# Performance work log

Hardware: AMD Instinct MI355X
Metric: run time of the kernel (lower is better)

Reference implementation:

```python
import jax, jax.numpy as jnp
import numpy as np

D = 6            # tree depth: 63 nodes per tree, leaves-first level order
HL = 256         # lstm hidden dim
HM = 128         # mlp hid dim
OFFSETS = [0, 32, 48, 56, 60, 62]  # level l occupies [off, off+2**(D-1-l))


def _lin(k, fan_in, fan_out, scale=0.02):
    return jax.random.normal(k, (fan_in, fan_out), jnp.float32) * scale


def setup_inputs() -> dict:
    key = jax.random.key(0)
    ks = jax.random.split(key, 40)
    B, N = 1024, 63
    inp = {
        "op": jax.random.normal(ks[0], (B, N, 32), jnp.float32),
        "feat": jax.random.normal(ks[1], (B, N, 64), jnp.float32),
        "cond1": jax.random.normal(ks[2], (B, N, 256), jnp.float32),
        "cond2": jax.random.normal(ks[3], (B, N, 256), jnp.float32),
        "bitmap": jax.random.uniform(ks[4], (B, N, 1000), jnp.float32),
        "has_cond": jnp.ones((B, N), jnp.float32),
        # embeddings (stored [in, out], i.e. transposed torch Linear weight)
        "W_op": _lin(ks[5], 32, HM), "b_op": jnp.zeros((HM,), jnp.float32),
        "W_feat": _lin(ks[6], 64, HM), "b_feat": jnp.zeros((HM,), jnp.float32),
        "W_pred": _lin(ks[7], 256, HM), "b_pred": jnp.zeros((HM,), jnp.float32),
        "W_bm": _lin(ks[8], 1000, HM), "b_bm": jnp.zeros((HM,), jnp.float32),
        # node LSTM (torch layout: [4*HL, in])
        "W_ih": jax.random.normal(ks[9], (4 * HL, 5 * HM), jnp.float32) * 0.02,
        "b_ih": jnp.zeros((4 * HL,), jnp.float32),
        "W_hh": jax.random.normal(ks[10], (4 * HL, HL), jnp.float32) * 0.02,
        "b_hh": jnp.zeros((4 * HL,), jnp.float32),
        # descendant attention
        "W_wh": _lin(ks[11], HL, 64), "W_ext": _lin(ks[12], 5 * HM, 64),
        "W_a": _lin(ks[13], 64, 1),
        "W_ht": _lin(ks[14], HL, HL), "b_ht": jnp.zeros((HL,), jnp.float32),
        # output heads
        "W_c1": _lin(ks[15], HL, HM), "b_c1": jnp.zeros((HM,), jnp.float32),
        "W_c2": _lin(ks[16], HM, HM), "b_c2": jnp.zeros((HM,), jnp.float32),
        "W_c3": _lin(ks[17], HM, 1), "b_c3": jnp.zeros((1,), jnp.float32),
        "W_d1": _lin(ks[18], HL, HM), "b_d1": jnp.zeros((HM,), jnp.float32),
        "W_d2": _lin(ks[19], HM, HM), "b_d2": jnp.zeros((HM,), jnp.float32),
        "W_d3": _lin(ks[20], HM, 1), "b_d3": jnp.zeros((1,), jnp.float32),
    }
    return inp


def _tree_forward(op, feat, cond1, cond2, bitmap, has_cond,
                  W_op, b_op, W_feat, b_feat, W_pred, b_pred, W_bm, b_bm,
                  W_ih, b_ih, W_hh, b_hh, W_wh, W_ext, W_a, W_ht, b_ht):
    B = op.shape[0]
    # per-node 5*HM input vector (conditions are single Compare predicates)
    x = jnp.concatenate([
        op @ W_op + b_op,
        feat @ W_feat + b_feat,
        cond1 @ W_pred + b_pred,
        cond2 @ W_pred + b_pred,
        (bitmap @ W_bm + b_bm) * has_cond[..., None],
    ], axis=-1)                                        # [B, 63, 5*HM]

    hiddens, cells = [], []
    for l in range(D):
        n, off = 2 ** (D - 1 - l), OFFSETS[l]
        xl = x[:, off:off + n]                         # [B, n, 5*HM]
        if l == 0:  # leaves: no children, no descendants
            h0 = jnp.zeros((B, n, HL), x.dtype)
            c0 = h0
        else:
            # all descendant hiddens of each node, grouped per parent
            desc = jnp.concatenate(
                [hiddens[lp].reshape(B, n, 2 ** (l - lp), HL) for lp in range(l)],
                axis=2)                                # [B, n, M, HL]
            e = jnp.tanh(desc @ W_wh + (xl @ W_ext)[:, :, None, :])
            logits = (e @ W_a)[..., 0]                 # [B, n, M]
            w = jax.nn.softmax(logits, axis=-1)        # exp/sum(exp)
            pooled = jnp.einsum('bnm,bnmh->bnh', w, desc)
            h0 = jnp.tanh(pooled @ W_ht + b_ht)        # hidden_transformation
            c0 = 0.5 * cells[l - 1].reshape(B, n, 2, HL).sum(axis=2)  # avg child cells
        # single-step LSTM (torch gate order i, f, g, o)
        gates = xl @ W_ih.T + b_ih + h0 @ W_hh.T + b_hh
        i_, f_, g_, o_ = jnp.split(gates, 4, axis=-1)
        c = jax.nn.sigmoid(f_) * c0 + jax.nn.sigmoid(i_) * jnp.tanh(g_)
        h = jax.nn.sigmoid(o_) * jnp.tanh(c)
        hiddens.append(h)
        cells.append(c)
    return hiddens[-1][:, 0]                           # root hidden [B, HL]


def reference(op, feat, cond1, cond2, bitmap, has_cond,
              W_op, b_op, W_feat, b_feat, W_pred, b_pred, W_bm, b_bm,
              W_ih, b_ih, W_hh, b_hh, W_wh, W_ext, W_a, W_ht, b_ht,
              W_c1, b_c1, W_c2, b_c2, W_c3, b_c3,
              W_d1, b_d1, W_d2, b_d2, W_d3, b_d3):
    root = _tree_forward(op, feat, cond1, cond2, bitmap, has_cond,
                         W_op, b_op, W_feat, b_feat, W_pred, b_pred, W_bm, b_bm,
                         W_ih, b_ih, W_hh, b_hh, W_wh, W_ext, W_a, W_ht, b_ht)
    cost = jax.nn.sigmoid(jax.nn.relu(jax.nn.relu(root @ W_c1 + b_c1) @ W_c2 + b_c2) @ W_c3 + b_c3)
    card = jax.nn.sigmoid(jax.nn.relu(jax.nn.relu(root @ W_d1 + b_d1) @ W_d2 + b_d2) @ W_d3 + b_d3)
    return (cost, card)
```

## Files before the change

kernel.cpp:

```cpp
#include <hip/hip_runtime.h>
#include <math.h>

typedef unsigned short u16;
typedef __bf16 bf16x8 __attribute__((ext_vector_type(8)));
typedef float f32x4 __attribute__((ext_vector_type(4)));

static __device__ __forceinline__ float sigf(float x){ return 1.0f/(1.0f+expf(-x)); }
static __device__ __forceinline__ u16 f2bf(float f){
    unsigned u = __builtin_bit_cast(unsigned, f);
    unsigned r = u + 0x7FFFu + ((u >> 16) & 1u);
    return (u16)(r >> 16);
}
static __device__ __forceinline__ float b2f(u16 s){
    unsigned u = ((unsigned)s) << 16;
    return __builtin_bit_cast(float, u);
}

__global__ void prep_w(const float* __restrict__ W, u16* __restrict__ Wt,
                       int K, int N, int Kpad)
{
    int idx = blockIdx.x * 256 + threadIdx.x;
    if (idx >= N * Kpad) return;
    int n = idx / Kpad, k = idx - n * Kpad;
    Wt[idx] = (k < K) ? f2bf(W[(long)k * N + n]) : (u16)0;
}

__global__ void prep_g(const float* __restrict__ W_ih, const float* __restrict__ W_hh,
                       u16* __restrict__ Wt)
{
    int idx = blockIdx.x * 256 + threadIdx.x;
    int n = idx / 896, k = idx - n * 896;
    float v = (k < 640) ? W_ih[(long)n * 640 + k] : W_hh[(long)n * 256 + (k - 640)];
    Wt[idx] = f2bf(v);
}

template<bool AF32, int BN>
__launch_bounds__(256)
__global__ void gemm_bf16(const void* __restrict__ Aptr, const u16* __restrict__ Bt,
                          void* __restrict__ Cout, const float* __restrict__ bias,
                          const float* __restrict__ rowscale,
                          int Kreal, int Kpad, int lda, int ldc,
                          int permA, int act, int outBF16)
{
    constexpr int BM = 128, LDT = 40;
    constexpr int WM = (BN == 128) ? 2 : 4;
    constexpr int MI = BM / WM / 16;
    constexpr int NI = (BN == 128) ? 4 : 4;
    __shared__ u16 As[BM * LDT];
    __shared__ u16 Bs[BN * LDT];

    const int tid = threadIdx.x;
    const int lane = tid & 63, wv = tid >> 6;
    const int r0 = blockIdx.x * BM, c0 = blockIdx.y * BN;
    const int wr = (wv % WM) * (BM / WM);
    const int wc = (wv / WM) * 64;
    const int l15 = lane & 15, q8 = (lane >> 4) * 8;

    f32x4 acc[MI][NI];
#pragma unroll
    for (int i = 0; i < MI; i++)
#pragma unroll
        for (int j = 0; j < NI; j++) acc[i][j] = (f32x4){0.f, 0.f, 0.f, 0.f};

    for (int kt = 0; kt < Kpad; kt += 32) {
        if (AF32) {
            const float* Ag = (const float*)Aptr;
#pragma unroll
            for (int p = 0; p < 4; p++) {
                int v = tid + p * 256;
                int row = v >> 3, kc = (v & 7) * 4;
                long ar = r0 + row;
                long arow = permA ? ((ar & 1023) * 63 + (ar >> 10)) : ar;
                int k = kt + kc;
                float4 val;
                if (k + 4 <= Kreal) {
                    val = *(const float4*)(Ag + arow * (long)lda + k);
                } else {
                    val.x = (k + 0 < Kreal) ? Ag[arow * (long)lda + k + 0] : 0.f;
                    val.y = (k + 1 < Kreal) ? Ag[arow * (long)lda + k + 1] : 0.f;
                    val.z = (k + 2 < Kreal) ? Ag[arow * (long)lda + k + 2] : 0.f;
                    val.w = (k + 3 < Kreal) ? Ag[arow * (long)lda + k + 3] : 0.f;
                }
                ushort4 o; o.x = f2bf(val.x); o.y = f2bf(val.y); o.z = f2bf(val.z); o.w = f2bf(val.w);
                *(ushort4*)&As[row * LDT + kc] = o;
            }
        } else {
            const u16* Ag = (const u16*)Aptr;
#pragma unroll
            for (int p = 0; p < 2; p++) {
                int v = tid + p * 256;
                int row = v >> 2, kc = (v & 3) * 8;
                long ar = r0 + row;
                *(int4*)&As[row * LDT + kc] = *(const int4*)(Ag + ar * (long)lda + kt + kc);
            }
        }
        constexpr int BCH = BN * 4 / 256;
#pragma unroll
        for (int p = 0; p < BCH; p++) {
            int v = tid + p * 256;
            int row = v >> 2, kc = (v & 3) * 8;
            *(int4*)&Bs[row * LDT + kc] = *(const int4*)(Bt + (long)(c0 + row) * Kpad + kt + kc);
        }
        __syncthreads();

        bf16x8 af[MI], bfr[NI];
#pragma unroll
        for (int mi = 0; mi < MI; mi++)
            af[mi] = *reinterpret_cast<const bf16x8*>(&As[(wr + mi * 16 + l15) * LDT + q8]);
#pragma unroll
        for (int ni = 0; ni < NI; ni++)
            bfr[ni] = *reinterpret_cast<const bf16x8*>(&Bs[(wc + ni * 16 + l15) * LDT + q8]);
#pragma unroll
        for (int mi = 0; mi < MI; mi++)
#pragma unroll
            for (int ni = 0; ni < NI; ni++)
                acc[mi][ni] = __builtin_amdgcn_mfma_f32_16x16x32_bf16(af[mi], bfr[ni], acc[mi][ni], 0, 0, 0);
        __syncthreads();
    }

#pragma unroll
    for (int mi = 0; mi < MI; mi++) {
#pragma unroll
        for (int ni = 0; ni < NI; ni++) {
#pragma unroll
            for (int r = 0; r < 4; r++) {
                int row = r0 + wr + mi * 16 + (lane >> 4) * 4 + r;
                int col = c0 + wc + ni * 16 + l15;
                float v = acc[mi][ni][r];
                if (bias) v += bias[col];
                if (act == 1) v = tanhf(v);
                if (rowscale) v *= rowscale[(row & 1023) * 63 + (row >> 10)];
                if (outBF16) ((u16*)Cout)[(long)row * ldc + col] = f2bf(v);
                else         ((float*)Cout)[(long)row * ldc + col] = v;
            }
        }
    }
}

__launch_bounds__(256)
__global__ void gates_mfma(const u16* __restrict__ xl, const u16* __restrict__ h0,
                           const u16* __restrict__ Wt_g,
                           const float* __restrict__ b_ih, const float* __restrict__ b_hh,
                           const float* __restrict__ Cprev,
                           u16* __restrict__ Hbuf, float* __restrict__ Cbuf,
                           int offCur, int offPrev, int Ktot)
{
    constexpr int LDT = 40;
    __shared__ u16 smem[128 * 136];
    __shared__ float bias_s[4][32];
    u16* As = smem;
    u16* Bs = smem + 128 * LDT;
    u16* Gs = smem;

    const int tid = threadIdx.x;
    const int lane = tid & 63, wv = tid >> 6;
    const int r0 = blockIdx.x * 128;
    const int by32 = blockIdx.y * 32;
    const int wr = (wv & 1) * 64, wc = (wv >> 1) * 64;
    const int l15 = lane & 15, q8 = (lane >> 4) * 8;

    if (tid < 128) {
        int g = tid >> 5, c = tid & 31;
        int gcol = g * 256 + by32 + c;
        bias_s[g][c] = b_ih[gcol] + b_hh[gcol];
    }

    f32x4 acc[4][4];
#pragma unroll
    for (int i = 0; i < 4; i++)
#pragma unroll
        for (int j = 0; j < 4; j++) acc[i][j] = (f32x4){0.f, 0.f, 0.f, 0.f};

    for (int kt = 0; kt < Ktot; kt += 32) {
#pragma unroll
        for (int p = 0; p < 2; p++) {
            int v = tid + p * 256;
            int row = v >> 2, kc = (v & 3) * 8;
            long ar = r0 + row;
            int k = kt + kc;
            int4 val;
            if (k < 640) val = *(const int4*)(xl + ar * 640L + k);
            else         val = *(const int4*)(h0 + ar * 256L + (k - 640));
            *(int4*)&As[row * LDT + kc] = val;
        }
#pragma unroll
        for (int p = 0; p < 2; p++) {
            int v = tid + p * 256;
            int row = v >> 2, kc = (v & 3) * 8;
            long brow = (long)((row >> 5) * 256 + by32 + (row & 31));
            *(int4*)&Bs[row * LDT + kc] = *(const int4*)(Wt_g + brow * 896 + kt + kc);
        }
        __syncthreads();

        bf16x8 af[4], bfr[4];
#pragma unroll
        for (int mi = 0; mi < 4; mi++)
            af[mi] = *reinterpret_cast<const bf16x8*>(&As[(wr + mi * 16 + l15) * LDT + q8]);
#pragma unroll
        for (int ni = 0; ni < 4; ni++)
            bfr[ni] = *reinterpret_cast<const bf16x8*>(&Bs[(wc + ni * 16 + l15) * LDT + q8]);
#pragma unroll
        for (int mi = 0; mi < 4; mi++)
#pragma unroll
            for (int ni = 0; ni < 4; ni++)
                acc[mi][ni] = __builtin_amdgcn_mfma_f32_16x16x32_bf16(af[mi], bfr[ni], acc[mi][ni], 0, 0, 0);
        __syncthreads();
    }

#pragma unroll
    for (int mi = 0; mi < 4; mi++)
#pragma unroll
        for (int ni = 0; ni < 4; ni++)
#pragma unroll
            for (int r = 0; r < 4; r++) {
                int lr = wr + mi * 16 + (lane >> 4) * 4 + r;
                int lc = wc + ni * 16 + l15;
                Gs[lr * 136 + lc] = f2bf(acc[mi][ni][r]);
            }
    __syncthreads();

#pragma unroll
    for (int i = 0; i < 16; i++) {
        int r = (tid >> 5) * 16 + i;
        int c = tid & 31;
        float iv = b2f(Gs[r * 136 + c])      + bias_s[0][c];
        float fv = b2f(Gs[r * 136 + 32 + c]) + bias_s[1][c];
        float gv = b2f(Gs[r * 136 + 64 + c]) + bias_s[2][c];
        float ov = b2f(Gs[r * 136 + 96 + c]) + bias_s[3][c];
        int rloc = r0 + r;
        int nd = rloc >> 10, bb = rloc & 1023;
        int gcol = by32 + c;
        float c0v = 0.f;
        if (Cprev) {
            long ch = ((long)(offPrev + nd * 2) * 1024 + bb) * 256 + gcol;
            c0v = 0.5f * (Cprev[ch] + Cprev[ch + 262144]);
        }
        float cv = sigf(fv) * c0v + sigf(iv) * tanhf(gv);
        float hv = sigf(ov) * tanhf(cv);
        long orow = ((long)offCur * 1024 + rloc) * 256 + gcol;
        Cbuf[orow] = cv;
        Hbuf[orow] = f2bf(hv);
    }
}

__launch_bounds__(256)
__global__ void attn_logits(const float* __restrict__ E, const float* __restrict__ xextall,
                            const float* __restrict__ W_a, float* __restrict__ Lbuf,
                            int level, int rows, int m, int off)
{
    const int wv = threadIdx.x >> 6, ln = threadIdx.x & 63;
    const long dr = (long)blockIdx.x * 4 + wv;
    if (dr >= rows) return;
    const int g = (int)(dr >> 10), bb = (int)(dr & 1023);
    int lp, node;
    if      (g < 32) { lp = 0; node = g;      }
    else if (g < 48) { lp = 1; node = g - 32; }
    else if (g < 56) { lp = 2; node = g - 48; }
    else if (g < 60) { lp = 3; node = g - 56; }
    else             { lp = 4; node = g - 60; }
    const int shift  = level - lp;
    const int i      = node >> shift;
    const int within = node & ((1 << shift) - 1);
    const int d      = ((2 << level) - (2 << shift)) + within;

    float e = E[dr * 64 + ln] + xextall[((long)(off + i) * 1024 + bb) * 64 + ln];
    float v = tanhf(e) * W_a[ln];
#pragma unroll
    for (int s = 32; s; s >>= 1) v += __shfl_xor(v, s);
    if (ln == 0) Lbuf[((long)(i * m + d)) * 1024 + bb] = v;
}

__launch_bounds__(256)
__global__ void attn_pool(const float* __restrict__ Lbuf, const u16* __restrict__ Hbuf,
                          float* __restrict__ pooled, int level, int m)
{
    const int blk = blockIdx.x;
    const int i = blk >> 10, bb = blk & 1023;
    const int tid = threadIdx.x;
    __shared__ float raw[64];
    __shared__ float wsm[64];
    if (tid < m) raw[tid] = Lbuf[((long)(i * m + tid)) * 1024 + bb];
    __syncthreads();
    if (tid == 0) {
        float mx = -1e30f;
        for (int d = 0; d < m; d++) mx = fmaxf(mx, raw[d]);
        float s = 0.f;
        for (int d = 0; d < m; d++) { float e = expf(raw[d] - mx); wsm[d] = e; s += e; }
        float inv = 1.f / s;
        for (int d = 0; d < m; d++) wsm[d] *= inv;
    }
    __syncthreads();
    float accv = 0.f;
    const int h = tid;
    int cum = 0;
    for (int lp = 0; lp < level; lp++) {
        int sz = 1 << (level - lp);
        int base = 64 - (64 >> lp);
        for (int q = 0; q < sz; q++) {
            long row = (long)(base + i * sz + q) * 1024 + bb;
            accv = fmaf(wsm[cum + q], b2f(Hbuf[row * 256 + h]), accv);
        }
        cum += sz;
    }
    pooled[(long)blk * 256 + h] = accv;
}

__launch_bounds__(256)
__global__ void heads_kernel(const u16* __restrict__ Hbuf,
                             const float* __restrict__ W_c1, const float* __restrict__ b_c1,
                             const float* __restrict__ W_c2, const float* __restrict__ b_c2,
                             const float* __restrict__ W_c3, const float* __restrict__ b_c3,
                             const float* __restrict__ W_d1, const float* __restrict__ b_d1,
                             const float* __restrict__ W_d2, const float* __restrict__ b_d2,
                             const float* __restrict__ W_d3, const float* __restrict__ b_d3,
                             float* __restrict__ out)
{
    const int bb = blockIdx.x, tid = threadIdx.x;
    __shared__ float root[256];
    __shared__ float t1[128];
    __shared__ float t2[128];
    __shared__ float red[256];
    root[tid] = b2f(Hbuf[((long)62 * 1024 + bb) * 256 + tid]);
    __syncthreads();
    for (int head = 0; head < 2; head++) {
        const float* w1  = head ? W_d1 : W_c1;
        const float* bi1 = head ? b_d1 : b_c1;
        const float* w2  = head ? W_d2 : W_c2;
        const float* bi2 = head ? b_d2 : b_c2;
        const float* w3  = head ? W_d3 : W_c3;
        const float* bi3 = head ? b_d3 : b_c3;
        if (tid < 128) {
            float s = bi1[tid];
            for (int k = 0; k < 256; k++) s = fmaf(root[k], w1[k * 128 + tid], s);
            t1[tid] = fmaxf(s, 0.f);
        }
        __syncthreads();
        if (tid < 128) {
            float s = bi2[tid];
            for (int k = 0; k < 128; k++) s = fmaf(t1[k], w2[k * 128 + tid], s);
            t2[tid] = fmaxf(s, 0.f);
        }
        __syncthreads();
        red[tid] = (tid < 128) ? t2[tid] * w3[tid] : 0.f;
        __syncthreads();
        for (int s = 128; s; s >>= 1) { if (tid < s) red[tid] += red[tid + s]; __syncthreads(); }
        if (tid == 0) out[head * 1024 + bb] = sigf(red[0] + bi3[0]);
        __syncthreads();
    }
}

extern "C" void kernel_launch(void* const* d_in, const int* in_sizes, int n_in,
                              void* d_out, int out_size, void* d_ws, size_t ws_size,
                              hipStream_t stream)
{
    (void)in_sizes; (void)n_in; (void)out_size;
    const float* op       = (const float*)d_in[0];
    const float* feat     = (const float*)d_in[1];
    const float* cond1    = (const float*)d_in[2];
    const float* cond2    = (const float*)d_in[3];
    const float* bitmap   = (const float*)d_in[4];
    const float* has_cond = (const float*)d_in[5];
    const float* W_op     = (const float*)d_in[6];
    const float* b_op     = (const float*)d_in[7];
    const float* W_feat   = (const float*)d_in[8];
    const float* b_feat   = (const float*)d_in[9];
    const float* W_pred   = (const float*)d_in[10];
    const float* b_pred   = (const float*)d_in[11];
    const float* W_bm     = (const float*)d_in[12];
    const float* b_bm     = (const float*)d_in[13];
    const float* W_ih     = (const float*)d_in[14];
    const float* b_ih     = (const float*)d_in[15];
    const float* W_hh     = (const float*)d_in[16];
    const float* b_hh     = (const float*)d_in[17];
    const float* W_wh     = (const float*)d_in[18];
    const float* W_ext    = (const float*)d_in[19];
    const float* W_a      = (const float*)d_in[20];
    const float* W_ht     = (const float*)d_in[21];
    const float* b_ht     = (const float*)d_in[22];
    const float* W_c1     = (const float*)d_in[23];
    const float* b_c1     = (const float*)d_in[24];
    const float* W_c2     = (const float*)d_in[25];
    const float* b_c2     = (const float*)d_in[26];
    const float* W_c3     = (const float*)d_in[27];
    const float* b_c3     = (const float*)d_in[28];
    const float* W_d1     = (const float*)d_in[29];
    const float* b_d1     = (const float*)d_in[30];
    const float* W_d2     = (const float*)d_in[31];
    const float* b_d2     = (const float*)d_in[32];
    const float* W_d3     = (const float*)d_in[33];
    const float* b_d3     = (const float*)d_in[34];
    float* out = (float*)d_out;

    char* p = (char*)d_ws;
    auto alloc = [&](size_t bytes) -> char* {
        char* r = p; p += (bytes + 255) & ~(size_t)255; return r;
    };
    u16*   xall    = (u16*)  alloc((size_t)64512 * 640 * 2);
    float* xextall = (float*)alloc((size_t)64512 * 64 * 4);
    u16*   Hbuf    = (u16*)  alloc((size_t)64512 * 256 * 2);
    float* Cbuf    = (float*)alloc((size_t)64512 * 256 * 4);
    float* Ebuf    = (float*)alloc((size_t)62 * 1024 * 64 * 4);
    float* pooled  = (float*)alloc((size_t)16384 * 256 * 4);
    u16*   h0      = (u16*)  alloc((size_t)16384 * 256 * 2);
    float* Lbuf    = (float*)alloc((size_t)65536 * 4);
    u16*   Wt_op   = (u16*)  alloc((size_t)128 * 32 * 2);
    u16*   Wt_feat = (u16*)  alloc((size_t)128 * 64 * 2);
    u16*   Wt_pred = (u16*)  alloc((size_t)128 * 256 * 2);
    u16*   Wt_bm   = (u16*)  alloc((size_t)128 * 1024 * 2);
    u16*   Wt_g    = (u16*)  alloc((size_t)1024 * 896 * 2);
    u16*   Wt_wh   = (u16*)  alloc((size_t)64 * 256 * 2);
    u16*   Wt_ext  = (u16*)  alloc((size_t)64 * 640 * 2);
    u16*   Wt_ht   = (u16*)  alloc((size_t)256 * 256 * 2);
    if (ws_size < (size_t)(p - (char*)d_ws)) return;

    prep_w<<<16,  256, 0, stream>>>(W_op,   Wt_op,   32,   128, 32);
    prep_w<<<32,  256, 0, stream>>>(W_feat, Wt_feat, 64,   128, 64);
    prep_w<<<128, 256, 0, stream>>>(W_pred, Wt_pred, 256,  128, 256);
    prep_w<<<512, 256, 0, stream>>>(W_bm,   Wt_bm,   1000, 128, 1024);
    prep_w<<<64,  256, 0, stream>>>(W_wh,   Wt_wh,   256,  64,  256);
    prep_w<<<160, 256, 0, stream>>>(W_ext,  Wt_ext,  640,  64,  640);
    prep_w<<<256, 256, 0, stream>>>(W_ht,   Wt_ht,   256,  256, 256);
    prep_g<<<3584,256, 0, stream>>>(W_ih, W_hh, Wt_g);

    gemm_bf16<true,128><<<dim3(504,1), 256, 0, stream>>>(op,     Wt_op,   (void*)(xall + 0),   b_op,   nullptr,  32,   32,   32,   640, 1, 0, 1);
    gemm_bf16<true,128><<<dim3(504,1), 256, 0, stream>>>(feat,   Wt_feat, (void*)(xall + 128), b_feat, nullptr,  64,   64,   64,   640, 1, 0, 1);
    gemm_bf16<true,128><<<dim3(504,1), 256, 0, stream>>>(cond1,  Wt_pred, (void*)(xall + 256), b_pred, nullptr,  256,  256,  256,  640, 1, 0, 1);
    gemm_bf16<true,128><<<dim3(504,1), 256, 0, stream>>>(cond2,  Wt_pred, (void*)(xall + 384), b_pred, nullptr,  256,  256,  256,  640, 1, 0, 1);
    gemm_bf16<true,128><<<dim3(504,1), 256, 0, stream>>>(bitmap, Wt_bm,   (void*)(xall + 512), b_bm,   has_cond, 1000, 1024, 1000, 640, 1, 0, 1);
    gemm_bf16<false,64><<<dim3(504,1), 256, 0, stream>>>(xall, Wt_ext, (void*)xextall, nullptr, nullptr, 640, 640, 640, 64, 0, 0, 0);

    for (int l = 0; l < 6; l++) {
        const int n   = 32 >> l;
        const int off = 64 - (64 >> l);
        const int M   = n * 1024;
        const int m   = (2 << l) - 2;

        if (l > 0) {
            int rows = off * 1024;
            attn_logits<<<rows / 4, 256, 0, stream>>>(Ebuf, xextall, W_a, Lbuf, l, rows, m, off);
            attn_pool<<<M, 256, 0, stream>>>(Lbuf, Hbuf, pooled, l, m);
            gemm_bf16<true,128><<<dim3(M/128, 2), 256, 0, stream>>>(pooled, Wt_ht, (void*)h0, b_ht, nullptr, 256, 256, 256, 256, 0, 1, 1);
        }

        const int Ktot    = l ? 896 : 640;
        const int offPrev = l ? (64 - (64 >> (l - 1))) : 0;
        gates_mfma<<<dim3(M/128, 8), 256, 0, stream>>>(xall + (size_t)off * 1024 * 640, h0, Wt_g,
                                                       b_ih, b_hh, l ? Cbuf : nullptr,
                                                       Hbuf, Cbuf, off, offPrev, Ktot);

        if (l < 5) {
            gemm_bf16<false,64><<<dim3(M/128, 1), 256, 0, stream>>>(Hbuf + (size_t)off * 1024 * 256, Wt_wh,
                                                                    (void*)(Ebuf + (size_t)off * 1024 * 64),
                                                                    nullptr, nullptr, 256, 256, 256, 64, 0, 0, 0);
        }
    }

    heads_kernel<<<1024, 256, 0, stream>>>(Hbuf, W_c1, b_c1, W_c2, b_c2, W_c3, b_c3,
                                           W_d1, b_d1, W_d2, b_d2, W_d3, b_d3, out);
}
```

Before: 1.396 ms.

## Use direct global-to-LDS loads in GEMMs and fuse attention logits with pooling

The gates GEMM and the bf16-input GEMMs that produce the attention projections now stage tiles with global_load_lds, writing straight into shared memory with no register round-trip. The tiles use an unpadded 32-element row stride, which may raise LDS bank conflicts on the fragment reads. Separately, the attention logits and softmax-pooling kernels are merged into one per-(node, batch) kernel that computes the logits, runs a wave-level softmax and pools, removing the Lbuf round-trip and one launch per level. The fused kernel recomputes the level-membership mapping in a small loop per descendant.

After: 1.316 ms. 5.7% less time.

```diff
diff --git a/kernel.cpp b/kernel.cpp
--- a/kernel.cpp
+++ b/kernel.cpp
@@ -14,6 +14,12 @@
 static __device__ __forceinline__ float b2f(u16 s){
     unsigned u = ((unsigned)s) << 16;
     return __builtin_bit_cast(float, u);
+}
+
+#define AS1 __attribute__((address_space(1)))
+#define AS3 __attribute__((address_space(3)))
+static __device__ __forceinline__ void gload16(const void* g, void* l){
+    __builtin_amdgcn_global_load_lds((const AS1 void*)g, (AS3 void*)l, 16, 0, 0);
 }
 
 __global__ void prep_w(const float* __restrict__ W, u16* __restrict__ Wt,
@@ -45,7 +51,7 @@
     constexpr int BM = 128, LDT = 40;
     constexpr int WM = (BN == 128) ? 2 : 4;
     constexpr int MI = BM / WM / 16;
-    constexpr int NI = (BN == 128) ? 4 : 4;
+    constexpr int NI = 4;
     __shared__ u16 As[BM * LDT];
     __shared__ u16 Bs[BN * LDT];
 
@@ -138,26 +144,88 @@
 }
 
 __launch_bounds__(256)
-__global__ void gates_mfma(const u16* __restrict__ xl, const u16* __restrict__ h0,
+__global__ void gemm_glds64(const u16* __restrict__ A, const u16* __restrict__ Bt,
+                            float* __restrict__ Cout, int Kpad, int lda, int ldc)
+{
+    __shared__ u16 As[128 * 32];
+    __shared__ u16 Bs[64 * 32];
+
+    const int tid = threadIdx.x;
+    const int lane = tid & 63, wv = tid >> 6;
+    const long r0 = (long)blockIdx.x * 128;
+    const int wr = wv * 32;
+    const int l15 = lane & 15, q8 = (lane >> 4) * 8;
+    const int crow = lane >> 2;
+    const int ckc  = (lane & 3) * 8;
+
+    f32x4 acc[2][4];
+#pragma unroll
+    for (int i = 0; i < 2; i++)
+#pragma unroll
+        for (int j = 0; j < 4; j++) acc[i][j] = (f32x4){0.f, 0.f, 0.f, 0.f};
+
+    for (int kt = 0; kt < Kpad; kt += 32) {
+#pragma unroll
+        for (int i = 0; i < 2; i++) {
+            int j = wv * 2 + i;
+            int row = j * 16 + crow;
+            gload16(A + (r0 + row) * lda + kt + ckc, &As[j * 512]);
+        }
+        {
+            int row = wv * 16 + crow;
+            gload16(Bt + (long)row * Kpad + kt + ckc, &Bs[wv * 512]);
+        }
+        __syncthreads();
+
+        bf16x8 af[2], bfr[4];
+#pragma unroll
+        for (int mi = 0; mi < 2; mi++)
+            af[mi] = *reinterpret_cast<const bf16x8*>(&As[(wr + mi * 16 + l15) * 32 + q8]);
+#pragma unroll
+        for (int ni = 0; ni < 4; ni++)
+            bfr[ni] = *reinterpret_cast<const bf16x8*>(&Bs[(ni * 16 + l15) * 32 + q8]);
+#pragma unroll
+        for (int mi = 0; mi < 2; mi++)
+#pragma unroll
+            for (int ni = 0; ni < 4; ni++)
+                acc[mi][ni] = __builtin_amdgcn_mfma_f32_16x16x32_bf16(af[mi], bfr[ni], acc[mi][ni], 0, 0, 0);
+        __syncthreads();
+    }
+
+#pragma unroll
+    for (int mi = 0; mi < 2; mi++)
+#pragma unroll
+        for (int ni = 0; ni < 4; ni++)
+#pragma unroll
+            for (int r = 0; r < 4; r++) {
+                long row = r0 + wr + mi * 16 + (lane >> 4) * 4 + r;
+                int col = ni * 16 + l15;
+                Cout[row * ldc + col] = acc[mi][ni][r];
+            }
+}
+
+__launch_bounds__(256)
+__global__ void gates_glds(const u16* __restrict__ xl, const u16* __restrict__ h0,
                            const u16* __restrict__ Wt_g,
                            const float* __restrict__ b_ih, const float* __restrict__ b_hh,
                            const float* __restrict__ Cprev,
                            u16* __restrict__ Hbuf, float* __restrict__ Cbuf,
                            int offCur, int offPrev, int Ktot)
 {
-    constexpr int LDT = 40;
     __shared__ u16 smem[128 * 136];
     __shared__ float bias_s[4][32];
     u16* As = smem;
-    u16* Bs = smem + 128 * LDT;
+    u16* Bs = smem + 4096;
     u16* Gs = smem;
 
     const int tid = threadIdx.x;
     const int lane = tid & 63, wv = tid >> 6;
-    const int r0 = blockIdx.x * 128;
+    const long r0 = (long)blockIdx.x * 128;
     const int by32 = blockIdx.y * 32;
     const int wr = (wv & 1) * 64, wc = (wv >> 1) * 64;
     const int l15 = lane & 15, q8 = (lane >> 4) * 8;
+    const int crow = lane >> 2;
+    const int ckc  = (lane & 3) * 8;
 
     if (tid < 128) {
         int g = tid >> 5, c = tid & 31;
@@ -173,32 +241,30 @@
 
     for (int kt = 0; kt < Ktot; kt += 32) {
 #pragma unroll
-        for (int p = 0; p < 2; p++) {
-            int v = tid + p * 256;
-            int row = v >> 2, kc = (v & 3) * 8;
+        for (int i = 0; i < 2; i++) {
+            int j = wv * 2 + i;
+            int row = j * 16 + crow;
             long ar = r0 + row;
-            int k = kt + kc;
-            int4 val;
-            if (k < 640) val = *(const int4*)(xl + ar * 640L + k);
-            else         val = *(const int4*)(h0 + ar * 256L + (k - 640));
-            *(int4*)&As[row * LDT + kc] = val;
-        }
-#pragma unroll
-        for (int p = 0; p < 2; p++) {
-            int v = tid + p * 256;
-            int row = v >> 2, kc = (v & 3) * 8;
+            int k = kt + ckc;
+            const u16* src = (kt < 640) ? (xl + ar * 640 + k) : (h0 + ar * 256 + (k - 640));
+            gload16(src, &As[j * 512]);
+        }
+#pragma unroll
+        for (int i = 0; i < 2; i++) {
+            int j = wv * 2 + i;
+            int row = j * 16 + crow;
             long brow = (long)((row >> 5) * 256 + by32 + (row & 31));
-            *(int4*)&Bs[row * LDT + kc] = *(const int4*)(Wt_g + brow * 896 + kt + kc);
+            gload16(Wt_g + brow * 896 + kt + ckc, &Bs[j * 512]);
         }
         __syncthreads();
 
         bf16x8 af[4], bfr[4];
 #pragma unroll
         for (int mi = 0; mi < 4; mi++)
-            af[mi] = *reinterpret_cast<const bf16x8*>(&As[(wr + mi * 16 + l15) * LDT + q8]);
+            af[mi] = *reinterpret_cast<const bf16x8*>(&As[(wr + mi * 16 + l15) * 32 + q8]);
 #pragma unroll
         for (int ni = 0; ni < 4; ni++)
-            bfr[ni] = *reinterpret_cast<const bf16x8*>(&Bs[(wc + ni * 16 + l15) * LDT + q8]);
+            bfr[ni] = *reinterpret_cast<const bf16x8*>(&Bs[(wc + ni * 16 + l15) * 32 + q8]);
 #pragma unroll
         for (int mi = 0; mi < 4; mi++)
 #pragma unroll
@@ -227,8 +293,8 @@
         float fv = b2f(Gs[r * 136 + 32 + c]) + bias_s[1][c];
         float gv = b2f(Gs[r * 136 + 64 + c]) + bias_s[2][c];
         float ov = b2f(Gs[r * 136 + 96 + c]) + bias_s[3][c];
-        int rloc = r0 + r;
-        int nd = rloc >> 10, bb = rloc & 1023;
+        long rloc = r0 + r;
+        int nd = (int)(rloc >> 10), bb = (int)(rloc & 1023);
         int gcol = by32 + c;
         float c0v = 0.f;
         if (Cprev) {
@@ -244,65 +310,60 @@
 }
 
 __launch_bounds__(256)
-__global__ void attn_logits(const float* __restrict__ E, const float* __restrict__ xextall,
-                            const float* __restrict__ W_a, float* __restrict__ Lbuf,
-                            int level, int rows, int m, int off)
-{
-    const int wv = threadIdx.x >> 6, ln = threadIdx.x & 63;
-    const long dr = (long)blockIdx.x * 4 + wv;
-    if (dr >= rows) return;
-    const int g = (int)(dr >> 10), bb = (int)(dr & 1023);
-    int lp, node;
-    if      (g < 32) { lp = 0; node = g;      }
-    else if (g < 48) { lp = 1; node = g - 32; }
-    else if (g < 56) { lp = 2; node = g - 48; }
-    else if (g < 60) { lp = 3; node = g - 56; }
-    else             { lp = 4; node = g - 60; }
-    const int shift  = level - lp;
-    const int i      = node >> shift;
-    const int within = node & ((1 << shift) - 1);
-    const int d      = ((2 << level) - (2 << shift)) + within;
-
-    float e = E[dr * 64 + ln] + xextall[((long)(off + i) * 1024 + bb) * 64 + ln];
-    float v = tanhf(e) * W_a[ln];
-#pragma unroll
-    for (int s = 32; s; s >>= 1) v += __shfl_xor(v, s);
-    if (ln == 0) Lbuf[((long)(i * m + d)) * 1024 + bb] = v;
-}
-
-__launch_bounds__(256)
-__global__ void attn_pool(const float* __restrict__ Lbuf, const u16* __restrict__ Hbuf,
-                          float* __restrict__ pooled, int level, int m)
+__global__ void attn_fused(const float* __restrict__ E, const float* __restrict__ xextall,
+                           const float* __restrict__ W_a, const u16* __restrict__ Hbuf,
+                           float* __restrict__ pooled, int level, int m, int off)
 {
     const int blk = blockIdx.x;
     const int i = blk >> 10, bb = blk & 1023;
     const int tid = threadIdx.x;
+    const int ln = tid & 63, wv = tid >> 6;
+    __shared__ float xs[64];
     __shared__ float raw[64];
     __shared__ float wsm[64];
-    if (tid < m) raw[tid] = Lbuf[((long)(i * m + tid)) * 1024 + bb];
+
+    if (tid < 64) xs[tid] = xextall[((long)(off + i) * 1024 + bb) * 64 + tid];
     __syncthreads();
-    if (tid == 0) {
-        float mx = -1e30f;
-        for (int d = 0; d < m; d++) mx = fmaxf(mx, raw[d]);
-        float s = 0.f;
-        for (int d = 0; d < m; d++) { float e = expf(raw[d] - mx); wsm[d] = e; s += e; }
-        float inv = 1.f / s;
-        for (int d = 0; d < m; d++) wsm[d] *= inv;
+
+    const float wa = W_a[ln];
+    for (int dd = wv; dd < m; dd += 4) {
+        int lp = 0, cum = 0;
+        for (;;) { int sz = 1 << (level - lp); if (dd < cum + sz) break; cum += sz; lp++; }
+        int sz = 1 << (level - lp);
+        int q = dd - cum;
+        long row = (long)((64 - (64 >> lp)) + i * sz + q) * 1024 + bb;
+        float v = tanhf(E[row * 64 + ln] + xs[ln]) * wa;
+#pragma unroll
+        for (int s = 32; s; s >>= 1) v += __shfl_xor(v, s);
+        if (ln == 0) raw[dd] = v;
     }
     __syncthreads();
+
+    if (tid < 64) {
+        float v = (tid < m) ? raw[tid] : -1e30f;
+        float mx = v;
+#pragma unroll
+        for (int s = 32; s; s >>= 1) mx = fmaxf(mx, __shfl_xor(mx, s));
+        float e = (tid < m) ? expf(v - mx) : 0.f;
+        float sum = e;
+#pragma unroll
+        for (int s = 32; s; s >>= 1) sum += __shfl_xor(sum, s);
+        wsm[tid] = e / sum;
+    }
+    __syncthreads();
+
     float accv = 0.f;
-    const int h = tid;
     int cum = 0;
     for (int lp = 0; lp < level; lp++) {
         int sz = 1 << (level - lp);
         int base = 64 - (64 >> lp);
         for (int q = 0; q < sz; q++) {
             long row = (long)(base + i * sz + q) * 1024 + bb;
-            accv = fmaf(wsm[cum + q], b2f(Hbuf[row * 256 + h]), accv);
+            accv = fmaf(wsm[cum + q], b2f(Hbuf[row * 256 + tid]), accv);
         }
         cum += sz;
     }
-    pooled[(long)blk * 256 + h] = accv;
+    pooled[(long)blk * 256 + tid] = accv;
 }
 
 __launch_bounds__(256)
@@ -402,7 +463,6 @@
     float* Ebuf    = (float*)alloc((size_t)62 * 1024 * 64 * 4);
     float* pooled  = (float*)alloc((size_t)16384 * 256 * 4);
     u16*   h0      = (u16*)  alloc((size_t)16384 * 256 * 2);
-    float* Lbuf    = (float*)alloc((size_t)65536 * 4);
     u16*   Wt_op   = (u16*)  alloc((size_t)128 * 32 * 2);
     u16*   Wt_feat = (u16*)  alloc((size_t)128 * 64 * 2);
     u16*   Wt_pred = (u16*)  alloc((size_t)128 * 256 * 2);
@@ -427,7 +487,7 @@
     gemm_bf16<true,128><<<dim3(504,1), 256, 0, stream>>>(cond1,  Wt_pred, (void*)(xall + 256), b_pred, nullptr,  256,  256,  256,  640, 1, 0, 1);
     gemm_bf16<true,128><<<dim3(504,1), 256, 0, stream>>>(cond2,  Wt_pred, (void*)(xall + 384), b_pred, nullptr,  256,  256,  256,  640, 1, 0, 1);
     gemm_bf16<true,128><<<dim3(504,1), 256, 0, stream>>>(bitmap, Wt_bm,   (void*)(xall + 512), b_bm,   has_cond, 1000, 1024, 1000, 640, 1, 0, 1);
-    gemm_bf16<false,64><<<dim3(504,1), 256, 0, stream>>>(xall, Wt_ext, (void*)xextall, nullptr, nullptr, 640, 640, 640, 64, 0, 0, 0);
+    gemm_glds64<<<504, 256, 0, stream>>>(xall, Wt_ext, xextall, 640, 640, 64);
 
     for (int l = 0; l < 6; l++) {
         const int n   = 32 >> l;
@@ -436,22 +496,19 @@
         const int m   = (2 << l) - 2;
 
         if (l > 0) {
-            int rows = off * 1024;
-            attn_logits<<<rows / 4, 256, 0, stream>>>(Ebuf, xextall, W_a, Lbuf, l, rows, m, off);
-            attn_pool<<<M, 256, 0, stream>>>(Lbuf, Hbuf, pooled, l, m);
+            attn_fused<<<M, 256, 0, stream>>>(Ebuf, xextall, W_a, Hbuf, pooled, l, m, off);
             gemm_bf16<true,128><<<dim3(M/128, 2), 256, 0, stream>>>(pooled, Wt_ht, (void*)h0, b_ht, nullptr, 256, 256, 256, 256, 0, 1, 1);
         }
 
         const int Ktot    = l ? 896 : 640;
         const int offPrev = l ? (64 - (64 >> (l - 1))) : 0;
-        gates_mfma<<<dim3(M/128, 8), 256, 0, stream>>>(xall + (size_t)off * 1024 * 640, h0, Wt_g,
+        gates_glds<<<dim3(M/128, 8), 256, 0, stream>>>(xall + (size_t)off * 1024 * 640, h0, Wt_g,
                                                        b_ih, b_hh, l ? Cbuf : nullptr,
                                                        Hbuf, Cbuf, off, offPrev, Ktot);
 
         if (l < 5) {
-            gemm_bf16<false,64><<<dim3(M/128, 1), 256, 0, stream>>>(Hbuf + (size_t)off * 1024 * 256, Wt_wh,
-                                                                    (void*)(Ebuf + (size_t)off * 1024 * 64),
-                                                                    nullptr, nullptr, 256, 256, 256, 64, 0, 0, 0);
+            gemm_glds64<<<M/128, 256, 0, stream>>>(Hbuf + (size_t)off * 1024 * 256, Wt_wh,
+                                                   Ebuf + (size_t)off * 1024 * 64, 256, 256, 64);
         }
     }
 
```
